# Kernel tuning notes

Measured on AMD Instinct MI355X. Metric: run time of the kernel, lower is better.

## Reference

```python
import jax, jax.numpy as jnp
import numpy as np

BN_EPS = 1e-5

def setup_inputs() -> dict:
    key = jax.random.key(0)
    ks = jax.random.split(key, 7)
    B, D, A = 16384, 768, 51
    s = 1.0 / np.sqrt(D)
    return {
        "x": jax.random.normal(ks[0], (B, D), dtype=jnp.float32),
        "W_embed": jax.random.uniform(ks[1], (D, D), minval=-s, maxval=s, dtype=jnp.float32),
        "b_embed": jax.random.uniform(ks[2], (D,), minval=-s, maxval=s, dtype=jnp.float32),
        "W_attr": jax.random.uniform(ks[3], (A, D), minval=-s, maxval=s, dtype=jnp.float32),  # stacked per-attribute (dim->1) heads
        "b_attr": jax.random.uniform(ks[4], (A,), minval=-s, maxval=s, dtype=jnp.float32),
        "gamma": jnp.ones((A,), dtype=jnp.float32),
        "beta": jnp.zeros((A,), dtype=jnp.float32),
    }

def reference(x, W_embed, b_embed, W_attr, b_attr, gamma, beta):
    # word_embed: Linear(dim, dim)
    h = x @ W_embed.T + b_embed                      # [B, D]
    # fused per-attribute heads: cat of attr_num (dim->1) linears == one (dim->attr_num) matmul
    logits = h @ W_attr.T + b_attr                    # [B, A]
    # BatchNorm1d (training mode: batch statistics, biased variance)
    mean = jnp.mean(logits, axis=0)
    var = jnp.var(logits, axis=0)
    y = (logits - mean) * jax.lax.rsqrt(var + BN_EPS) * gamma + beta
    return y
```

## Files before the change

### kernel.cpp

```cpp
#include <hip/hip_runtime.h>
#include <hip/hip_bf16.h>

typedef _Float16 halfx8 __attribute__((ext_vector_type(8)));
typedef _Float16 halfx4 __attribute__((ext_vector_type(4)));
typedef float floatx4 __attribute__((ext_vector_type(4)));

#define GLOBAL_AS __attribute__((address_space(1)))
#define LDS_AS __attribute__((address_space(3)))

__device__ __forceinline__ void async_copy_16(const void* g, void* l) {
    __builtin_amdgcn_global_load_lds((GLOBAL_AS void*)g, (LDS_AS void*)l, 16, 0, 0);
}

#define PM 16384
#define PD 768
#define PA 51


__global__ __launch_bounds__(192) void precompute_kernel(
    const float* __restrict__ We, const float* __restrict__ Wa,
    const float* __restrict__ b_embed, const float* __restrict__ b_attr,
    _Float16* __restrict__ wc16, float* __restrict__ bc, float* __restrict__ stats)
{
    int b = blockIdx.x, t = threadIdx.x;
    if (b < PA) {
        int d0 = t * 4;
        const float* war = Wa + (size_t)b * PD;
        float a0 = 0.f, a1 = 0.f, a2 = 0.f, a3 = 0.f;
        #pragma unroll 8
        for (int k = 0; k < PD; ++k) {
            float w = war[k];
            floatx4 v = *(const floatx4*)(We + (size_t)k * PD + d0);
            a0 += w * v[0]; a1 += w * v[1]; a2 += w * v[2]; a3 += w * v[3];
        }
        halfx4 h;
        h[0] = (_Float16)a0; h[1] = (_Float16)a1; h[2] = (_Float16)a2; h[3] = (_Float16)a3;
        *(halfx4*)(wc16 + (size_t)b * PD + d0) = h;
    } else if (b == PA) {
        halfx8 z;
        #pragma unroll
        for (int j = 0; j < 8; ++j) z[j] = (_Float16)0.f;
        for (int i = t; i < 1248; i += 192)
            *(halfx8*)(wc16 + PA * PD + i * 8) = z;
        if (t < 128) stats[t] = 0.f;
    } else {
        if (t < PA) {
            const float* war = Wa + (size_t)t * PD;
            float acc = 0.f;
            #pragma unroll 4
            for (int k = 0; k < PD; k += 4) {
                floatx4 w = *(const floatx4*)(war + k);
                floatx4 e = *(const floatx4*)(b_embed + k);
                acc += w[0] * e[0] + w[1] * e[1] + w[2] * e[2] + w[3] * e[3];
            }
            bc[t] = acc + b_attr[t];
        }
    }
}

__global__ __launch_bounds__(256) void skinny_gemm_kernel(
    const float* __restrict__ X,
    const _Float16* __restrict__ Wc,
    const float* __restrict__ bc,
    float* __restrict__ logits,
    float* __restrict__ stats)
{
    __shared__ float As[64 * 64];
    __shared__ _Float16 Bs[64 * 64];
    __shared__ float s_sum[64];
    __shared__ float s_ssq[64];

    const int tid = threadIdx.x;
    const int wave = tid >> 6;
    const int lane = tid & 63;
    const int quad = lane >> 4;
    const int l16 = lane & 15;
    const int row0 = blockIdx.x * 64;

    if (tid < 64) { s_sum[tid] = 0.f; s_ssq[tid] = 0.f; }

    const int a_r  = lane >> 4;
    const int a_sl = lane & 15;
    const int b_r  = lane >> 3;
    const int b_sl = lane & 7;

    floatx4 acc[4];
    #pragma unroll
    for (int j = 0; j < 4; ++j) acc[j] = (floatx4){0.f, 0.f, 0.f, 0.f};

    for (int kt = 0; kt < PD; kt += 64) {
        #pragma unroll
        for (int j = 0; j < 4; ++j) {
            int g = wave * 4 + j;
            int r = g * 4 + a_r;
            int c = a_sl ^ (r & 7);
            async_copy_16(X + (size_t)(row0 + r) * PD + kt + c * 4, &As[g * 256]);
        }
        #pragma unroll
        for (int j = 0; j < 2; ++j) {
            int g = wave * 2 + j;
            int r = g * 8 + b_r;
            int c = b_sl ^ (r & 7);
            async_copy_16(Wc + (size_t)r * PD + kt + c * 8, &Bs[g * 512]);
        }
        __syncthreads();
        #pragma unroll
        for (int ks = 0; ks < 2; ++ks) {
            int r = wave * 16 + l16;
            int c0 = ks * 8 + quad * 2;
            floatx4 p0 = *(const floatx4*)&As[r * 64 + ((c0 ^ (l16 & 7)) << 2)];
            floatx4 p1 = *(const floatx4*)&As[r * 64 + (((c0 + 1) ^ (l16 & 7)) << 2)];
            halfx8 af;
            af[0] = (_Float16)p0[0]; af[1] = (_Float16)p0[1];
            af[2] = (_Float16)p0[2]; af[3] = (_Float16)p0[3];
            af[4] = (_Float16)p1[0]; af[5] = (_Float16)p1[1];
            af[6] = (_Float16)p1[2]; af[7] = (_Float16)p1[3];
            halfx8 bf[4];
            #pragma unroll
            for (int ni = 0; ni < 4; ++ni)
                bf[ni] = *(const halfx8*)&Bs[(ni * 16 + l16) * 64 +
                                             (((ks * 4 + quad) ^ (l16 & 7)) << 3)];
            #pragma unroll
            for (int ni = 0; ni < 4; ++ni)
                acc[ni] = __builtin_amdgcn_mfma_f32_16x16x32_f16(af, bf[ni], acc[ni], 0, 0, 0);
        }
        __syncthreads();
    }

    #pragma unroll
    for (int ni = 0; ni < 4; ++ni) {
        int col = ni * 16 + l16;
        if (col < PA) {
            float bv = bc[col];
            float ps = 0.f, pss = 0.f;
            int rowb = row0 + wave * 16 + quad * 4;
            #pragma unroll
            for (int r = 0; r < 4; ++r) {
                float v = acc[ni][r] + bv;
                logits[(size_t)(rowb + r) * PA + col] = v;
                ps += v; pss += v * v;
            }
            atomicAdd(&s_sum[col], ps);
            atomicAdd(&s_ssq[col], pss);
        }
    }
    __syncthreads();
    if (tid < PA) {
        atomicAdd(&stats[tid], s_sum[tid]);
        atomicAdd(&stats[64 + tid], s_ssq[tid]);
    }
}

__global__ void bn_finalize_kernel(const float* __restrict__ logits,
                                   const float* __restrict__ stats,
                                   const float* __restrict__ gamma,
                                   const float* __restrict__ beta,
                                   float* __restrict__ out, int total) {
    __shared__ float s_scale[PA];
    __shared__ float s_shift[PA];
    int t = threadIdx.x;
    if (t < PA) {
        const float invB = 1.0f / (float)PM;
        float mean = stats[t] * invB;
        float var = stats[64 + t] * invB - mean * mean;
        float inv = rsqrtf(var + 1e-5f);
        float g = gamma[t] * inv;
        s_scale[t] = g;
        s_shift[t] = beta[t] - mean * g;
    }
    __syncthreads();
    int idx = blockIdx.x * 256 + t;
    if (idx < total) {
        int col = idx % PA;
        out[idx] = logits[idx] * s_scale[col] + s_shift[col];
    }
}

extern "C" void kernel_launch(void* const* d_in, const int* in_sizes, int n_in,
                              void* d_out, int out_size, void* d_ws, size_t ws_size,
                              hipStream_t stream) {
    const float* x       = (const float*)d_in[0];
    const float* W_embed = (const float*)d_in[1];
    const float* b_embed = (const float*)d_in[2];
    const float* W_attr  = (const float*)d_in[3];
    const float* b_attr  = (const float*)d_in[4];
    const float* gamma   = (const float*)d_in[5];
    const float* beta    = (const float*)d_in[6];
    float* out = (float*)d_out;

    char* ws = (char*)d_ws;
    _Float16* wc16   = (_Float16*)(ws);
    float*    bc     = (float*)   (ws + 98304);
    float*    stats  = (float*)   (ws + 98560);
    float*    logits = (float*)   (ws + 99072);

    precompute_kernel<<<53, 192, 0, stream>>>(W_embed, W_attr, b_embed, b_attr, wc16, bc, stats);
    skinny_gemm_kernel<<<256, 256, 0, stream>>>(x, wc16, bc, logits, stats);
    bn_finalize_kernel<<<3264, 256, 0, stream>>>(logits, stats, gamma, beta, out, PM * PA);
}
```

Baseline: 152.2 us.

## Split-K tiled weight combine and smaller skinny GEMM row tiles

The combined weight Wc = Wa·We was computed by only 51 blocks, each looping serially over all 768 K values. It is now a separate kernel of 192 blocks that stage tiles in LDS and accumulate split-K partials into an fp32 buffer with atomics, after a zeroing init kernel. The skinny GEMM now processes 32 rows per block (512 blocks) with a 2x2 wave split and reads fp32 Wc, converting to fp16 in registers. This adds a kernel launch, atomic traffic and extra conversions in the GEMM in exchange for far more parallelism in the precompute.

```diff
diff --git a/kernel.cpp b/kernel.cpp
--- a/kernel.cpp
+++ b/kernel.cpp
@@ -17,56 +17,96 @@
 #define PA 51
 
 
-__global__ __launch_bounds__(192) void precompute_kernel(
-    const float* __restrict__ We, const float* __restrict__ Wa,
-    const float* __restrict__ b_embed, const float* __restrict__ b_attr,
-    _Float16* __restrict__ wc16, float* __restrict__ bc, float* __restrict__ stats)
+__global__ __launch_bounds__(256) void init_kernel(
+    const float* __restrict__ Wa, const float* __restrict__ b_embed,
+    const float* __restrict__ b_attr,
+    float* __restrict__ wc32, float* __restrict__ bc, float* __restrict__ stats)
 {
     int b = blockIdx.x, t = threadIdx.x;
-    if (b < PA) {
-        int d0 = t * 4;
-        const float* war = Wa + (size_t)b * PD;
-        float a0 = 0.f, a1 = 0.f, a2 = 0.f, a3 = 0.f;
-        #pragma unroll 8
-        for (int k = 0; k < PD; ++k) {
-            float w = war[k];
-            floatx4 v = *(const floatx4*)(We + (size_t)k * PD + d0);
-            a0 += w * v[0]; a1 += w * v[1]; a2 += w * v[2]; a3 += w * v[3];
-        }
-        halfx4 h;
-        h[0] = (_Float16)a0; h[1] = (_Float16)a1; h[2] = (_Float16)a2; h[3] = (_Float16)a3;
-        *(halfx4*)(wc16 + (size_t)b * PD + d0) = h;
-    } else if (b == PA) {
-        halfx8 z;
-        #pragma unroll
-        for (int j = 0; j < 8; ++j) z[j] = (_Float16)0.f;
-        for (int i = t; i < 1248; i += 192)
-            *(halfx8*)(wc16 + PA * PD + i * 8) = z;
+    if (b < 12) {
+        #pragma unroll
+        for (int j = 0; j < 4; ++j)
+            ((float4*)wc32)[b * 1024 + j * 256 + t] = (float4){0.f, 0.f, 0.f, 0.f};
+    } else {
         if (t < 128) stats[t] = 0.f;
-    } else {
-        if (t < PA) {
-            const float* war = Wa + (size_t)t * PD;
+        __shared__ float red[256];
+        int a = t & 63, qtr = t >> 6;
+        float partial = 0.f;
+        if (a < PA) {
+            const float* war = Wa + (size_t)a * PD + qtr * 192;
+            const float* ber = b_embed + qtr * 192;
+            #pragma unroll 4
+            for (int k = 0; k < 192; k += 4) {
+                floatx4 w = *(const floatx4*)(war + k);
+                floatx4 e = *(const floatx4*)(ber + k);
+                partial += w[0]*e[0] + w[1]*e[1] + w[2]*e[2] + w[3]*e[3];
+            }
+        }
+        red[t] = partial;
+        __syncthreads();
+        if (t < PA)
+            bc[t] = red[t] + red[64 + t] + red[128 + t] + red[192 + t] + b_attr[t];
+    }
+}
+
+__global__ __launch_bounds__(256) void wcomb_kernel(
+    const float* __restrict__ We, const float* __restrict__ Wa,
+    float* __restrict__ wc32)
+{
+    __shared__ float WeS[48 * 64];
+    __shared__ float WaS[51 * 48];
+    const int b = blockIdx.x;
+    const int kc = b & 15;
+    const int nc = b >> 4;
+    const int k0 = kc * 48, d0 = nc * 64;
+    const int t = threadIdx.x;
+
+    #pragma unroll
+    for (int j = 0; j < 3; ++j) {
+        int idx4 = j * 256 + t;
+        int r = idx4 >> 4, c4 = idx4 & 15;
+        *(floatx4*)&WeS[r * 64 + c4 * 4] =
+            *(const floatx4*)(We + (size_t)(k0 + r) * PD + d0 + c4 * 4);
+    }
+    for (int idx4 = t; idx4 < 612; idx4 += 256) {
+        int r = idx4 / 12, c4 = idx4 % 12;
+        *(floatx4*)&WaS[r * 48 + c4 * 4] =
+            *(const floatx4*)(Wa + (size_t)r * PD + k0 + c4 * 4);
+    }
+    __syncthreads();
+
+    const int c = t & 63;
+    const int ag = t >> 6;
+
+    float we[48];
+    #pragma unroll
+    for (int k = 0; k < 48; ++k) we[k] = WeS[k * 64 + c];
+
+    #pragma unroll
+    for (int i = 0; i < 13; ++i) {
+        int a = ag + i * 4;
+        if (a < PA) {
             float acc = 0.f;
-            #pragma unroll 4
-            for (int k = 0; k < PD; k += 4) {
-                floatx4 w = *(const floatx4*)(war + k);
-                floatx4 e = *(const floatx4*)(b_embed + k);
-                acc += w[0] * e[0] + w[1] * e[1] + w[2] * e[2] + w[3] * e[3];
-            }
-            bc[t] = acc + b_attr[t];
+            #pragma unroll
+            for (int k4 = 0; k4 < 12; ++k4) {
+                floatx4 wa = *(const floatx4*)&WaS[a * 48 + k4 * 4];
+                acc += wa[0] * we[k4*4] + wa[1] * we[k4*4+1]
+                     + wa[2] * we[k4*4+2] + wa[3] * we[k4*4+3];
+            }
+            atomicAdd(&wc32[(size_t)a * PD + d0 + c], acc);
         }
     }
 }
 
 __global__ __launch_bounds__(256) void skinny_gemm_kernel(
     const float* __restrict__ X,
-    const _Float16* __restrict__ Wc,
+    const float* __restrict__ Wc,
     const float* __restrict__ bc,
     float* __restrict__ logits,
     float* __restrict__ stats)
 {
-    __shared__ float As[64 * 64];
-    __shared__ _Float16 Bs[64 * 64];
+    __shared__ float As[32 * 64];
+    __shared__ float Bs[64 * 64];
     __shared__ float s_sum[64];
     __shared__ float s_ssq[64];
 
@@ -75,65 +115,70 @@
     const int lane = tid & 63;
     const int quad = lane >> 4;
     const int l16 = lane & 15;
-    const int row0 = blockIdx.x * 64;
+    const int wr = wave & 1;
+    const int wn = wave >> 1;
+    const int row0 = blockIdx.x * 32;
 
     if (tid < 64) { s_sum[tid] = 0.f; s_ssq[tid] = 0.f; }
 
-    const int a_r  = lane >> 4;
-    const int a_sl = lane & 15;
-    const int b_r  = lane >> 3;
-    const int b_sl = lane & 7;
-
-    floatx4 acc[4];
-    #pragma unroll
-    for (int j = 0; j < 4; ++j) acc[j] = (floatx4){0.f, 0.f, 0.f, 0.f};
+    const int g_r  = lane >> 4;
+    const int g_sl = lane & 15;
+
+    floatx4 acc[2];
+    acc[0] = (floatx4){0.f, 0.f, 0.f, 0.f};
+    acc[1] = (floatx4){0.f, 0.f, 0.f, 0.f};
 
     for (int kt = 0; kt < PD; kt += 64) {
+        #pragma unroll
+        for (int j = 0; j < 2; ++j) {
+            int g = wave * 2 + j;
+            int r = g * 4 + g_r;
+            int csrc = g_sl ^ (r & 7);
+            async_copy_16(X + (size_t)(row0 + r) * PD + kt + csrc * 4, &As[g * 256]);
+        }
         #pragma unroll
         for (int j = 0; j < 4; ++j) {
             int g = wave * 4 + j;
-            int r = g * 4 + a_r;
-            int c = a_sl ^ (r & 7);
-            async_copy_16(X + (size_t)(row0 + r) * PD + kt + c * 4, &As[g * 256]);
-        }
-        #pragma unroll
-        for (int j = 0; j < 2; ++j) {
-            int g = wave * 2 + j;
-            int r = g * 8 + b_r;
-            int c = b_sl ^ (r & 7);
-            async_copy_16(Wc + (size_t)r * PD + kt + c * 8, &Bs[g * 512]);
+            int r = g * 4 + g_r;
+            int csrc = g_sl ^ (r & 7);
+            async_copy_16(Wc + (size_t)r * PD + kt + csrc * 4, &Bs[g * 256]);
         }
         __syncthreads();
         #pragma unroll
         for (int ks = 0; ks < 2; ++ks) {
-            int r = wave * 16 + l16;
             int c0 = ks * 8 + quad * 2;
-            floatx4 p0 = *(const floatx4*)&As[r * 64 + ((c0 ^ (l16 & 7)) << 2)];
-            floatx4 p1 = *(const floatx4*)&As[r * 64 + (((c0 + 1) ^ (l16 & 7)) << 2)];
+            int sw = l16 & 7;
+            int rA = wr * 16 + l16;
+            floatx4 p0 = *(const floatx4*)&As[rA * 64 + ((c0 ^ sw) << 2)];
+            floatx4 p1 = *(const floatx4*)&As[rA * 64 + (((c0 + 1) ^ sw) << 2)];
             halfx8 af;
             af[0] = (_Float16)p0[0]; af[1] = (_Float16)p0[1];
             af[2] = (_Float16)p0[2]; af[3] = (_Float16)p0[3];
             af[4] = (_Float16)p1[0]; af[5] = (_Float16)p1[1];
             af[6] = (_Float16)p1[2]; af[7] = (_Float16)p1[3];
-            halfx8 bf[4];
             #pragma unroll
-            for (int ni = 0; ni < 4; ++ni)
-                bf[ni] = *(const halfx8*)&Bs[(ni * 16 + l16) * 64 +
-                                             (((ks * 4 + quad) ^ (l16 & 7)) << 3)];
-            #pragma unroll
-            for (int ni = 0; ni < 4; ++ni)
-                acc[ni] = __builtin_amdgcn_mfma_f32_16x16x32_f16(af, bf[ni], acc[ni], 0, 0, 0);
+            for (int ni = 0; ni < 2; ++ni) {
+                int rB = wn * 32 + ni * 16 + l16;
+                floatx4 q0 = *(const floatx4*)&Bs[rB * 64 + ((c0 ^ sw) << 2)];
+                floatx4 q1 = *(const floatx4*)&Bs[rB * 64 + (((c0 + 1) ^ sw) << 2)];
+                halfx8 bf;
+                bf[0] = (_Float16)q0[0]; bf[1] = (_Float16)q0[1];
+                bf[2] = (_Float16)q0[2]; bf[3] = (_Float16)q0[3];
+                bf[4] = (_Float16)q1[0]; bf[5] = (_Float16)q1[1];
+                bf[6] = (_Float16)q1[2]; bf[7] = (_Float16)q1[3];
+                acc[ni] = __builtin_amdgcn_mfma_f32_16x16x32_f16(af, bf, acc[ni], 0, 0, 0);
+            }
         }
         __syncthreads();
     }
 
     #pragma unroll
-    for (int ni = 0; ni < 4; ++ni) {
-        int col = ni * 16 + l16;
+    for (int ni = 0; ni < 2; ++ni) {
+        int col = wn * 32 + ni * 16 + l16;
         if (col < PA) {
             float bv = bc[col];
             float ps = 0.f, pss = 0.f;
-            int rowb = row0 + wave * 16 + quad * 4;
+            int rowb = row0 + wr * 16 + quad * 4;
             #pragma unroll
             for (int r = 0; r < 4; ++r) {
                 float v = acc[ni][r] + bv;
@@ -189,12 +234,13 @@
     float* out = (float*)d_out;
 
     char* ws = (char*)d_ws;
-    _Float16* wc16   = (_Float16*)(ws);
-    float*    bc     = (float*)   (ws + 98304);
-    float*    stats  = (float*)   (ws + 98560);
-    float*    logits = (float*)   (ws + 99072);
-
-    precompute_kernel<<<53, 192, 0, stream>>>(W_embed, W_attr, b_embed, b_attr, wc16, bc, stats);
-    skinny_gemm_kernel<<<256, 256, 0, stream>>>(x, wc16, bc, logits, stats);
+    float* wc32   = (float*)(ws);
+    float* bc     = (float*)(ws + 196608);
+    float* stats  = (float*)(ws + 196864);
+    float* logits = (float*)(ws + 197376);
+
+    init_kernel<<<13, 256, 0, stream>>>(W_attr, b_embed, b_attr, wc32, bc, stats);
+    wcomb_kernel<<<192, 256, 0, stream>>>(W_embed, W_attr, wc32);
+    skinny_gemm_kernel<<<512, 256, 0, stream>>>(x, wc32, bc, logits, stats);
     bn_finalize_kernel<<<3264, 256, 0, stream>>>(logits, stats, gamma, beta, out, PM * PA);
 }
```

After: 131.3 us. 1.16x faster.
